# Kernel optimization log

Hardware: AMD Instinct MI355X
Metric: run time of the kernel (lower is better)

Reference implementation:

```python
import jax, jax.numpy as jnp
import numpy as np

NUM_EMBEDDINGS = 1024
DIM_EMBEDDING = 256
COMMITMENT_COST = 0.25


def setup_inputs() -> dict:
    key = jax.random.key(0)
    k1, k2 = jax.random.split(key)
    inputs = jax.random.normal(k1, (64, DIM_EMBEDDING, 32, 32), dtype=jnp.float32)
    # torch init: uniform(-1/K, 1/K)
    w = jax.random.uniform(k2, (NUM_EMBEDDINGS, DIM_EMBEDDING), dtype=jnp.float32,
                           minval=-1.0 / NUM_EMBEDDINGS, maxval=1.0 / NUM_EMBEDDINGS)
    return {"inputs": inputs, "w": w}


def reference(inputs, w):
    # NCHW -> NHWC
    x = jnp.transpose(inputs, (0, 2, 3, 1))            # [B,H,W,D]
    input_shape = x.shape
    flat = x.reshape(-1, DIM_EMBEDDING)                # [N,D]

    distances = (jnp.sum(flat * flat, axis=1, keepdims=True)
                 - 2.0 * jnp.matmul(flat, w.T)
                 + jnp.sum(w * w, axis=1))

    encoding_indices = jnp.argmax(-distances, axis=1)[:, None]      # [N,1] int
    encodings = jax.nn.one_hot(encoding_indices[:, 0], NUM_EMBEDDINGS,
                               dtype=jnp.float32)                   # [N,K]

    # gather instead of one-hot matmul (same math)
    quantized = jnp.take(w, encoding_indices[:, 0], axis=0)          # [N,D]
    quantized = quantized.reshape(input_shape)                       # [B,H,W,D]

    e_latent_loss = jnp.mean((jax.lax.stop_gradient(quantized) - x) ** 2)
    q_latent_loss = jnp.mean((quantized - jax.lax.stop_gradient(x)) ** 2)
    vq_loss = q_latent_loss + COMMITMENT_COST * e_latent_loss

    # straight-through estimator
    quantized_st = x + jax.lax.stop_gradient(quantized - x)
    quantized_out = jnp.transpose(quantized_st, (0, 3, 1, 2))        # NHWC -> NCHW

    avg_probs = jnp.mean(encodings, axis=0)
    perplexity = jnp.exp(-jnp.sum(avg_probs * jnp.log(avg_probs + 1e-10)))

    return (distances, quantized_out, vq_loss, encodings, encoding_indices, perplexity)
```

## Files before the change

### kernel.cpp

```cpp
#include <hip/hip_runtime.h>

#define N_TOT   65536
#define K_EMB   1024
#define D_EMB   256
#define HW      1024
#define CHW     (D_EMB * HW)

#define O_DIST  0
#define O_Q     67108864
#define O_LOSS  83886080
#define O_ENC   83886081
#define O_IDX   150994945
#define O_PPL   151060481

#define WS_CNT   0
#define WS_LOSSP 4096
#define WS_XX    6144
#define WS_WW    268288
#define WS_IDX   272384

__global__ __launch_bounds__(256) void k_xx(const float* __restrict__ in,
                                            float* __restrict__ xx) {
  int n = blockIdx.x * 256 + threadIdx.x;
  int b = n >> 10, hw = n & 1023;
  const float* p = in + (size_t)b * CHW + hw;
  float s = 0.f;
  #pragma unroll 8
  for (int d = 0; d < D_EMB; ++d) { float v = p[(size_t)d * HW]; s += v * v; }
  xx[n] = s;
}

__global__ __launch_bounds__(256) void k_ww(const float* __restrict__ w,
                                            float* __restrict__ ww) {
  int k = blockIdx.x * 256 + threadIdx.x;
  const float* p = w + (size_t)k * D_EMB;
  float s = 0.f;
  #pragma unroll 8
  for (int d = 0; d < D_EMB; ++d) { float v = p[d]; s += v * v; }
  ww[k] = s;
}

__global__ __launch_bounds__(256) void k_gemm(const float* __restrict__ in,
                                              const float* __restrict__ w,
                                              const float* __restrict__ xx,
                                              const float* __restrict__ ww,
                                              float* __restrict__ dist,
                                              int* __restrict__ aidx) {
  __shared__ __align__(16) float xs[32][68];
  __shared__ __align__(16) float wsh[32][68];
  __shared__ float rbest[64][16];
  __shared__ int   ridx[64][16];

  const int tid = threadIdx.x;
  const int tx = tid & 15, ty = tid >> 4;
  const int n0 = blockIdx.x * 64;
  const int b = n0 >> 10, hw0 = n0 & 1023;
  const float* xbase = in + (size_t)b * CHW + hw0;

  float best[4]; int bestk[4];
  #pragma unroll
  for (int i = 0; i < 4; ++i) { best[i] = 3.4e38f; bestk[i] = 0; }

  const int xr = tid >> 6;
  const int xc = tid & 63;
  const int wk = tid >> 3;
  const int wd = (tid & 7) * 4;

  for (int k0 = 0; k0 < K_EMB; k0 += 64) {
    float acc[4][4];
    #pragma unroll
    for (int i = 0; i < 4; ++i)
      #pragma unroll
      for (int j = 0; j < 4; ++j) acc[i][j] = 0.f;

    for (int d0 = 0; d0 < D_EMB; d0 += 32) {
      __syncthreads();
      #pragma unroll
      for (int it = 0; it < 8; ++it) {
        int dl = it * 4 + xr;
        xs[dl][xc] = xbase[(size_t)(d0 + dl) * HW + xc];
      }
      #pragma unroll
      for (int p = 0; p < 2; ++p) {
        int kl = p * 32 + wk;
        float4 v = *(const float4*)&w[(size_t)(k0 + kl) * D_EMB + d0 + wd];
        wsh[wd + 0][kl] = v.x; wsh[wd + 1][kl] = v.y;
        wsh[wd + 2][kl] = v.z; wsh[wd + 3][kl] = v.w;
      }
      __syncthreads();
      #pragma unroll
      for (int dd = 0; dd < 32; ++dd) {
        float4 xv = *(const float4*)&xs[dd][ty * 4];
        float4 wv = *(const float4*)&wsh[dd][tx * 4];
        acc[0][0] += xv.x * wv.x; acc[0][1] += xv.x * wv.y;
        acc[0][2] += xv.x * wv.z; acc[0][3] += xv.x * wv.w;
        acc[1][0] += xv.y * wv.x; acc[1][1] += xv.y * wv.y;
        acc[1][2] += xv.y * wv.z; acc[1][3] += xv.y * wv.w;
        acc[2][0] += xv.z * wv.x; acc[2][1] += xv.z * wv.y;
        acc[2][2] += xv.z * wv.z; acc[2][3] += xv.z * wv.w;
        acc[3][0] += xv.w * wv.x; acc[3][1] += xv.w * wv.y;
        acc[3][2] += xv.w * wv.z; acc[3][3] += xv.w * wv.w;
      }
    }
    float4 wwv = *(const float4*)&ww[k0 + tx * 4];
    #pragma unroll
    for (int i = 0; i < 4; ++i) {
      int nl = ty * 4 + i;
      float xxv = xx[n0 + nl];
      float4 o;
      o.x = xxv - 2.f * acc[i][0] + wwv.x;
      o.y = xxv - 2.f * acc[i][1] + wwv.y;
      o.z = xxv - 2.f * acc[i][2] + wwv.z;
      o.w = xxv - 2.f * acc[i][3] + wwv.w;
      *(float4*)&dist[(size_t)(n0 + nl) * K_EMB + k0 + tx * 4] = o;
      float dv[4] = {o.x, o.y, o.z, o.w};
      #pragma unroll
      for (int j = 0; j < 4; ++j) {
        if (dv[j] < best[i]) { best[i] = dv[j]; bestk[i] = k0 + tx * 4 + j; }
      }
    }
  }
  #pragma unroll
  for (int i = 0; i < 4; ++i) {
    rbest[ty * 4 + i][tx] = best[i];
    ridx[ty * 4 + i][tx] = bestk[i];
  }
  __syncthreads();
  if (tid < 64) {
    float bb = rbest[tid][0]; int bk = ridx[tid][0];
    #pragma unroll
    for (int t = 1; t < 16; ++t) {
      float v = rbest[tid][t]; int kk = ridx[tid][t];
      if (v < bb || (v == bb && kk < bk)) { bb = v; bk = kk; }
    }
    aidx[n0 + tid] = bk;
  }
}

__global__ __launch_bounds__(256) void k_epi(const float* __restrict__ in,
                                             const float* __restrict__ w,
                                             const int* __restrict__ aidx,
                                             float* __restrict__ outq,
                                             float* __restrict__ enc,
                                             float* __restrict__ idxf,
                                             int* __restrict__ cnt,
                                             double* __restrict__ lossp) {
  __shared__ double sred[256];
  int tid = threadIdx.x;
  int n = blockIdx.x * 256 + tid;
  int b = n >> 10, hw = n & 1023;
  int idx = aidx[n];
  const float* xp = in + (size_t)b * CHW + hw;
  float* qp = outq + (size_t)b * CHW + hw;
  const float* wrow = w + (size_t)idx * D_EMB;
  double ls = 0.0;
  #pragma unroll 4
  for (int d = 0; d < D_EMB; ++d) {
    float xv = xp[(size_t)d * HW];
    float q = wrow[d];
    float t = q - xv;
    qp[(size_t)d * HW] = xv + t;
    float sq = t * t;
    ls += (double)sq;
  }
  enc[(size_t)n * K_EMB + idx] = 1.0f;
  idxf[n] = (float)idx;
  atomicAdd(&cnt[idx], 1);
  sred[tid] = ls; __syncthreads();
  for (int s = 128; s > 0; s >>= 1) {
    if (tid < s) sred[tid] += sred[tid + s];
    __syncthreads();
  }
  if (tid == 0) lossp[blockIdx.x] = sred[0];
}

__global__ __launch_bounds__(256) void k_final(const double* __restrict__ lossp,
                                               const int* __restrict__ cnt,
                                               float* __restrict__ out_loss,
                                               float* __restrict__ out_ppl) {
  __shared__ double sred[256];
  int t = threadIdx.x;
  sred[t] = lossp[t];
  __syncthreads();
  for (int s = 128; s > 0; s >>= 1) {
    if (t < s) sred[t] += sred[t + s];
    __syncthreads();
  }
  if (t == 0) *out_loss = (float)(1.25 * (sred[0] / 16777216.0));
  __syncthreads();
  double es = 0.0;
  for (int k = t; k < K_EMB; k += 256) {
    float p = (float)cnt[k] * (1.0f / 65536.0f);
    float term = p * logf(p + 1e-10f);
    es += (double)term;
  }
  sred[t] = es;
  __syncthreads();
  for (int s = 128; s > 0; s >>= 1) {
    if (t < s) sred[t] += sred[t + s];
    __syncthreads();
  }
  if (t == 0) *out_ppl = expf((float)(-sred[0]));
}

extern "C" void kernel_launch(void* const* d_in, const int* in_sizes, int n_in,
                              void* d_out, int out_size, void* d_ws, size_t ws_size,
                              hipStream_t stream) {
  const float* in = (const float*)d_in[0];
  const float* w  = (const float*)d_in[1];
  float* out = (float*)d_out;
  char* ws = (char*)d_ws;

  int*    cnt   = (int*)(ws + WS_CNT);
  double* lossp = (double*)(ws + WS_LOSSP);
  float*  xx    = (float*)(ws + WS_XX);
  float*  wwp   = (float*)(ws + WS_WW);
  int*    aidx  = (int*)(ws + WS_IDX);

  hipMemsetAsync(cnt, 0, 4096, stream);
  hipMemsetAsync(out + O_ENC, 0, (size_t)67108864 * 4, stream);

  k_xx  <<<256, 256, 0, stream>>>(in, xx);
  k_ww  <<<4,   256, 0, stream>>>(w, wwp);
  k_gemm<<<1024, 256, 0, stream>>>(in, w, xx, wwp, out + O_DIST, aidx);
  k_epi <<<256, 256, 0, stream>>>(in, w, aidx, out + O_Q, out + O_ENC,
                                  out + O_IDX, cnt, lossp);
  k_final<<<1, 256, 0, stream>>>(lossp, cnt, out + O_LOSS, out + O_PPL);
}
```

Before: 1.200 ms.

## Use fp16 MFMA coarse distance GEMM with fp32 candidate re-evaluation for argmin

Converts inputs and codebook to fp16 (codebook scaled by 1024) in prep kernels and computes distances with v_mfma_f32_16x16x32_f16 using global_load_lds double-buffered staging. Per row, it records near-minimum candidates within a margin, then an fp32 re-evaluation kernel picks the exact argmin among them, falling back to a full scan on overflow. The epilogue now writes the full one-hot rows directly, which removes the large memset, and it reuses the encodings output region as scratch for the fp16 copies. The distances output now carries fp16-level error, which could affect tolerance.

```diff
diff --git a/kernel.cpp b/kernel.cpp
--- a/kernel.cpp
+++ b/kernel.cpp
@@ -1,4 +1,5 @@
 #include <hip/hip_runtime.h>
+#include <hip/hip_fp16.h>
 
 #define N_TOT   65536
 #define K_EMB   1024
@@ -15,157 +16,286 @@
 
 #define WS_CNT   0
 #define WS_LOSSP 4096
-#define WS_XX    6144
-#define WS_WW    268288
-#define WS_IDX   272384
-
-__global__ __launch_bounds__(256) void k_xx(const float* __restrict__ in,
-                                            float* __restrict__ xx) {
+#define WS_XX    12288
+#define WS_WW    274432
+#define WS_AIDX  278528
+
+#define CAP     15
+#define MARGIN  3.0e-4f
+
+typedef float  f32x4  __attribute__((ext_vector_type(4)));
+typedef short  short8 __attribute__((ext_vector_type(8)));
+typedef unsigned short ushort8 __attribute__((ext_vector_type(8)));
+typedef f32x4 __attribute__((aligned(4))) f32x4u;
+
+static __device__ __forceinline__ void gload16(const void* g, void* l) {
+  __builtin_amdgcn_global_load_lds(
+      (const __attribute__((address_space(1))) unsigned int*)g,
+      (__attribute__((address_space(3))) unsigned int*)l, 16, 0, 0);
+}
+
+__global__ __launch_bounds__(256) void k_prep_x(const float* __restrict__ in,
+                                                unsigned short* __restrict__ x2,
+                                                float* __restrict__ xx) {
   int n = blockIdx.x * 256 + threadIdx.x;
   int b = n >> 10, hw = n & 1023;
   const float* p = in + (size_t)b * CHW + hw;
-  float s = 0.f;
-  #pragma unroll 8
-  for (int d = 0; d < D_EMB; ++d) { float v = p[(size_t)d * HW]; s += v * v; }
-  xx[n] = s;
-}
-
-__global__ __launch_bounds__(256) void k_ww(const float* __restrict__ w,
-                                            float* __restrict__ ww) {
+  float hsum[2];
+  #pragma unroll
+  for (int half = 0; half < 2; ++half) {
+    float r[8];
+    for (int i = 0; i < 128; i += 8) {
+      ushort8 hv;
+      #pragma unroll
+      for (int j = 0; j < 8; ++j) {
+        int d = half * 128 + i + j;
+        float v = p[(size_t)d * HW];
+        float sq = v * v;
+        asm volatile("" : "+v"(sq));
+        if (i == 0) r[j] = sq; else r[j] += sq;
+        hv[j] = __half_as_ushort(__float2half_rn(v));
+      }
+      *(ushort8*)&x2[(size_t)n * 256 + half * 128 + i] = hv;
+    }
+    hsum[half] = ((r[0] + r[1]) + (r[2] + r[3])) + ((r[4] + r[5]) + (r[6] + r[7]));
+  }
+  xx[n] = hsum[0] + hsum[1];
+}
+
+__global__ __launch_bounds__(256) void k_prep_w(const float* __restrict__ w,
+                                                unsigned short* __restrict__ w2,
+                                                float* __restrict__ ww) {
   int k = blockIdx.x * 256 + threadIdx.x;
   const float* p = w + (size_t)k * D_EMB;
-  float s = 0.f;
-  #pragma unroll 8
-  for (int d = 0; d < D_EMB; ++d) { float v = p[d]; s += v * v; }
-  ww[k] = s;
-}
-
-__global__ __launch_bounds__(256) void k_gemm(const float* __restrict__ in,
+  float hsum[2];
+  #pragma unroll
+  for (int half = 0; half < 2; ++half) {
+    float r[8];
+    for (int i = 0; i < 128; i += 8) {
+      ushort8 hv;
+      #pragma unroll
+      for (int j = 0; j < 8; ++j) {
+        float v = p[half * 128 + i + j];
+        float sq = v * v;
+        asm volatile("" : "+v"(sq));
+        if (i == 0) r[j] = sq; else r[j] += sq;
+        hv[j] = __half_as_ushort(__float2half_rn(v * 1024.f));
+      }
+      *(ushort8*)&w2[(size_t)k * 256 + half * 128 + i] = hv;
+    }
+    hsum[half] = ((r[0] + r[1]) + (r[2] + r[3])) + ((r[4] + r[5]) + (r[6] + r[7]));
+  }
+  ww[k] = hsum[0] + hsum[1];
+}
+
+__global__ __launch_bounds__(512) void k_coarse(const unsigned short* __restrict__ x2,
+                                                const unsigned short* __restrict__ w2,
+                                                const float* __restrict__ xx,
+                                                const float* __restrict__ ww,
+                                                float* __restrict__ dist,
+                                                unsigned short* __restrict__ cand) {
+  __shared__ __align__(16) short As[2][4096];
+  __shared__ __align__(16) short Bs[2][4096];
+  __shared__ unsigned rowprov[128];
+  __shared__ unsigned rowcnt[128];
+  __shared__ unsigned short rowcand[128][CAP];
+
+  const int tid = threadIdx.x;
+  const int l = tid & 63, v = tid >> 6;
+  const int n0 = blockIdx.x * 128;
+  const int qr = v >> 1, qc = v & 1;
+
+  if (tid < 128) { rowprov[tid] = 0x7F800000u; rowcnt[tid] = 0u; }
+
+  float xv[2][4];
+  #pragma unroll
+  for (int m = 0; m < 2; ++m)
+    #pragma unroll
+    for (int r = 0; r < 4; ++r)
+      xv[m][r] = xx[n0 + qr * 32 + m * 16 + (l >> 4) * 4 + r];
+
+  const int srcrow = tid >> 2, srcoff = (tid & 3) * 16;
+
+  #define STAGE(buf, u) do {                                                   \
+    int k0_ = ((u) >> 3) * 128, d0_ = ((u) & 7) * 32;                          \
+    gload16((const char*)x2 + (size_t)(n0 + srcrow) * 512 + d0_ * 2 + srcoff,  \
+            (char*)As[buf] + v * 1024);                                        \
+    gload16((const char*)w2 + (size_t)(k0_ + srcrow) * 512 + d0_ * 2 + srcoff, \
+            (char*)Bs[buf] + v * 1024);                                        \
+  } while (0)
+
+  f32x4 acc[2][4];
+  int cur = 0;
+  STAGE(0, 0);
+  __syncthreads();
+
+  for (int u = 0; u < 64; ++u) {
+    if ((u & 7) == 0) {
+      #pragma unroll
+      for (int m = 0; m < 2; ++m)
+        #pragma unroll
+        for (int n = 0; n < 4; ++n) acc[m][n] = (f32x4){0.f, 0.f, 0.f, 0.f};
+    }
+    if (u < 63) STAGE(cur ^ 1, u + 1);
+
+    short8 af[2], bfr[4];
+    #pragma unroll
+    for (int m = 0; m < 2; ++m)
+      af[m] = *(const short8*)((const char*)As[cur] +
+                               (qr * 32 + m * 16 + (l & 15)) * 64 + (l >> 4) * 16);
+    #pragma unroll
+    for (int n = 0; n < 4; ++n)
+      bfr[n] = *(const short8*)((const char*)Bs[cur] +
+                                (qc * 64 + n * 16 + (l & 15)) * 64 + (l >> 4) * 16);
+    #pragma unroll
+    for (int m = 0; m < 2; ++m)
+      #pragma unroll
+      for (int n = 0; n < 4; ++n)
+        asm("v_mfma_f32_16x16x32_f16 %0, %1, %2, %0"
+            : "+v"(acc[m][n]) : "v"(af[m]), "v"(bfr[n]));
+
+    if ((u & 7) == 7) {
+      const int k0 = (u >> 3) * 128;
+      float wv[4];
+      float rmin[2][4];
+      #pragma unroll
+      for (int m = 0; m < 2; ++m)
+        #pragma unroll
+        for (int r = 0; r < 4; ++r) rmin[m][r] = 3.4e38f;
+      #pragma unroll
+      for (int n = 0; n < 4; ++n) {
+        const int kg = k0 + qc * 64 + n * 16 + (l & 15);
+        wv[n] = ww[kg];
+        #pragma unroll
+        for (int m = 0; m < 2; ++m)
+          #pragma unroll
+          for (int r = 0; r < 4; ++r) {
+            const int rl = qr * 32 + m * 16 + (l >> 4) * 4 + r;
+            float dd = (xv[m][r] - acc[m][n][r] * (1.f / 512.f)) + wv[n];
+            dist[(size_t)(n0 + rl) * 1024 + kg] = dd;
+            rmin[m][r] = fminf(rmin[m][r], dd);
+          }
+      }
+      #pragma unroll
+      for (int off = 1; off < 16; off <<= 1)
+        #pragma unroll
+        for (int m = 0; m < 2; ++m)
+          #pragma unroll
+          for (int r = 0; r < 4; ++r)
+            rmin[m][r] = fminf(rmin[m][r], __shfl_xor(rmin[m][r], off));
+      if ((l & 15) == 0) {
+        #pragma unroll
+        for (int m = 0; m < 2; ++m)
+          #pragma unroll
+          for (int r = 0; r < 4; ++r)
+            atomicMin(&rowprov[qr * 32 + m * 16 + (l >> 4) * 4 + r],
+                      __float_as_uint(rmin[m][r]));
+      }
+      __syncthreads();
+      #pragma unroll
+      for (int n = 0; n < 4; ++n) {
+        const int kg = k0 + qc * 64 + n * 16 + (l & 15);
+        #pragma unroll
+        for (int m = 0; m < 2; ++m)
+          #pragma unroll
+          for (int r = 0; r < 4; ++r) {
+            const int rl = qr * 32 + m * 16 + (l >> 4) * 4 + r;
+            float dd = (xv[m][r] - acc[m][n][r] * (1.f / 512.f)) + wv[n];
+            if (dd < __uint_as_float(rowprov[rl]) + MARGIN) {
+              unsigned slot = atomicAdd(&rowcnt[rl], 1u);
+              if (slot < CAP) rowcand[rl][slot] = (unsigned short)kg;
+            }
+          }
+      }
+    }
+    __syncthreads();
+    cur ^= 1;
+  }
+
+  if (tid < 128) {
+    unsigned c = rowcnt[tid];
+    unsigned short* dst = cand + (size_t)(n0 + tid) * 16;
+    dst[0] = (c > CAP) ? (unsigned short)0xFFFF : (unsigned short)c;
+    #pragma unroll
+    for (int i = 0; i < CAP; ++i) dst[1 + i] = rowcand[tid][i];
+  }
+  #undef STAGE
+}
+
+__global__ __launch_bounds__(256) void k_reeval(const float* __restrict__ in,
+                                                const float* __restrict__ w,
+                                                const float* __restrict__ xx,
+                                                const float* __restrict__ ww,
+                                                const unsigned short* __restrict__ cand,
+                                                int* __restrict__ aidx) {
+  int n = blockIdx.x * 256 + threadIdx.x;
+  int b = n >> 10, hw = n & 1023;
+  const unsigned short* c = cand + (size_t)n * 16;
+  int cnt = c[0];
+  int best;
+  if (cnt == 1) {
+    best = c[1];
+  } else {
+    const float* xp = in + (size_t)b * CHW + hw;
+    const float xxv = xx[n];
+    float bd = 3.4e38f; int bk = 1 << 30;
+    const bool full = (cnt > CAP);
+    const int m = full ? K_EMB : cnt;
+    for (int i = 0; i < m; ++i) {
+      int k = full ? i : (int)c[1 + i];
+      const float* wr = w + (size_t)k * D_EMB;
+      float acc = 0.f;
+      for (int d = 0; d < D_EMB; ++d)
+        acc = fmaf(xp[(size_t)d * HW], wr[d], acc);
+      float t = 2.0f * acc;
+      asm volatile("" : "+v"(t));
+      float s = xxv - t;
+      asm volatile("" : "+v"(s));
+      float dd = s + ww[k];
+      if (dd < bd || (dd == bd && k < bk)) { bd = dd; bk = k; }
+    }
+    best = bk;
+  }
+  aidx[n] = best;
+}
+
+__global__ __launch_bounds__(256) void k_epi2(const float* __restrict__ in,
                                               const float* __restrict__ w,
-                                              const float* __restrict__ xx,
-                                              const float* __restrict__ ww,
-                                              float* __restrict__ dist,
-                                              int* __restrict__ aidx) {
-  __shared__ __align__(16) float xs[32][68];
-  __shared__ __align__(16) float wsh[32][68];
-  __shared__ float rbest[64][16];
-  __shared__ int   ridx[64][16];
-
+                                              const int* __restrict__ aidx,
+                                              float* __restrict__ outq,
+                                              float* __restrict__ enc,
+                                              float* __restrict__ idxf,
+                                              int* __restrict__ cnt,
+                                              double* __restrict__ lossp) {
+  __shared__ double sred[256];
+  __shared__ int sidx[64];
   const int tid = threadIdx.x;
-  const int tx = tid & 15, ty = tid >> 4;
+  const int rr = tid & 63, qd = tid >> 6;
   const int n0 = blockIdx.x * 64;
-  const int b = n0 >> 10, hw0 = n0 & 1023;
-  const float* xbase = in + (size_t)b * CHW + hw0;
-
-  float best[4]; int bestk[4];
-  #pragma unroll
-  for (int i = 0; i < 4; ++i) { best[i] = 3.4e38f; bestk[i] = 0; }
-
-  const int xr = tid >> 6;
-  const int xc = tid & 63;
-  const int wk = tid >> 3;
-  const int wd = (tid & 7) * 4;
-
-  for (int k0 = 0; k0 < K_EMB; k0 += 64) {
-    float acc[4][4];
-    #pragma unroll
-    for (int i = 0; i < 4; ++i)
-      #pragma unroll
-      for (int j = 0; j < 4; ++j) acc[i][j] = 0.f;
-
-    for (int d0 = 0; d0 < D_EMB; d0 += 32) {
-      __syncthreads();
-      #pragma unroll
-      for (int it = 0; it < 8; ++it) {
-        int dl = it * 4 + xr;
-        xs[dl][xc] = xbase[(size_t)(d0 + dl) * HW + xc];
-      }
-      #pragma unroll
-      for (int p = 0; p < 2; ++p) {
-        int kl = p * 32 + wk;
-        float4 v = *(const float4*)&w[(size_t)(k0 + kl) * D_EMB + d0 + wd];
-        wsh[wd + 0][kl] = v.x; wsh[wd + 1][kl] = v.y;
-        wsh[wd + 2][kl] = v.z; wsh[wd + 3][kl] = v.w;
-      }
-      __syncthreads();
-      #pragma unroll
-      for (int dd = 0; dd < 32; ++dd) {
-        float4 xv = *(const float4*)&xs[dd][ty * 4];
-        float4 wv = *(const float4*)&wsh[dd][tx * 4];
-        acc[0][0] += xv.x * wv.x; acc[0][1] += xv.x * wv.y;
-        acc[0][2] += xv.x * wv.z; acc[0][3] += xv.x * wv.w;
-        acc[1][0] += xv.y * wv.x; acc[1][1] += xv.y * wv.y;
-        acc[1][2] += xv.y * wv.z; acc[1][3] += xv.y * wv.w;
-        acc[2][0] += xv.z * wv.x; acc[2][1] += xv.z * wv.y;
-        acc[2][2] += xv.z * wv.z; acc[2][3] += xv.z * wv.w;
-        acc[3][0] += xv.w * wv.x; acc[3][1] += xv.w * wv.y;
-        acc[3][2] += xv.w * wv.z; acc[3][3] += xv.w * wv.w;
-      }
-    }
-    float4 wwv = *(const float4*)&ww[k0 + tx * 4];
-    #pragma unroll
-    for (int i = 0; i < 4; ++i) {
-      int nl = ty * 4 + i;
-      float xxv = xx[n0 + nl];
-      float4 o;
-      o.x = xxv - 2.f * acc[i][0] + wwv.x;
-      o.y = xxv - 2.f * acc[i][1] + wwv.y;
-      o.z = xxv - 2.f * acc[i][2] + wwv.z;
-      o.w = xxv - 2.f * acc[i][3] + wwv.w;
-      *(float4*)&dist[(size_t)(n0 + nl) * K_EMB + k0 + tx * 4] = o;
-      float dv[4] = {o.x, o.y, o.z, o.w};
-      #pragma unroll
-      for (int j = 0; j < 4; ++j) {
-        if (dv[j] < best[i]) { best[i] = dv[j]; bestk[i] = k0 + tx * 4 + j; }
-      }
-    }
-  }
-  #pragma unroll
-  for (int i = 0; i < 4; ++i) {
-    rbest[ty * 4 + i][tx] = best[i];
-    ridx[ty * 4 + i][tx] = bestk[i];
-  }
-  __syncthreads();
-  if (tid < 64) {
-    float bb = rbest[tid][0]; int bk = ridx[tid][0];
-    #pragma unroll
-    for (int t = 1; t < 16; ++t) {
-      float v = rbest[tid][t]; int kk = ridx[tid][t];
-      if (v < bb || (v == bb && kk < bk)) { bb = v; bk = kk; }
-    }
-    aidx[n0 + tid] = bk;
-  }
-}
-
-__global__ __launch_bounds__(256) void k_epi(const float* __restrict__ in,
-                                             const float* __restrict__ w,
-                                             const int* __restrict__ aidx,
-                                             float* __restrict__ outq,
-                                             float* __restrict__ enc,
-                                             float* __restrict__ idxf,
-                                             int* __restrict__ cnt,
-                                             double* __restrict__ lossp) {
-  __shared__ double sred[256];
-  int tid = threadIdx.x;
-  int n = blockIdx.x * 256 + tid;
-  int b = n >> 10, hw = n & 1023;
-  int idx = aidx[n];
+  const int n = n0 + rr;
+  const int b = n >> 10, hw = n & 1023;
+  if (qd == 0) sidx[rr] = aidx[n];
+  __syncthreads();
+  const int idx = sidx[rr];
   const float* xp = in + (size_t)b * CHW + hw;
   float* qp = outq + (size_t)b * CHW + hw;
   const float* wrow = w + (size_t)idx * D_EMB;
   double ls = 0.0;
-  #pragma unroll 4
-  for (int d = 0; d < D_EMB; ++d) {
-    float xv = xp[(size_t)d * HW];
+  for (int j = 0; j < 64; ++j) {
+    int d = qd * 64 + j;
+    float xvv = xp[(size_t)d * HW];
     float q = wrow[d];
-    float t = q - xv;
-    qp[(size_t)d * HW] = xv + t;
-    float sq = t * t;
-    ls += (double)sq;
-  }
-  enc[(size_t)n * K_EMB + idx] = 1.0f;
-  idxf[n] = (float)idx;
-  atomicAdd(&cnt[idx], 1);
+    float t = q - xvv;
+    qp[(size_t)d * HW] = xvv + t;
+    ls += (double)(t * t);
+  }
+  if (qd == 0) { idxf[n] = (float)idx; atomicAdd(&cnt[idx], 1); }
+  for (int it = 0; it < 64; ++it) {
+    int ii = sidx[it];
+    f32x4 z = {0.f, 0.f, 0.f, 0.f};
+    if ((ii >> 2) == tid) z[ii & 3] = 1.f;
+    *(f32x4u*)&enc[(size_t)(n0 + it) * 1024 + tid * 4] = z;
+  }
   sred[tid] = ls; __syncthreads();
   for (int s = 128; s > 0; s >>= 1) {
     if (tid < s) sred[tid] += sred[tid + s];
@@ -180,7 +310,7 @@
                                                float* __restrict__ out_ppl) {
   __shared__ double sred[256];
   int t = threadIdx.x;
-  sred[t] = lossp[t];
+  sred[t] = lossp[t] + lossp[t + 256] + lossp[t + 512] + lossp[t + 768];
   __syncthreads();
   for (int s = 128; s > 0; s >>= 1) {
     if (t < s) sred[t] += sred[t + s];
@@ -215,15 +345,19 @@
   double* lossp = (double*)(ws + WS_LOSSP);
   float*  xx    = (float*)(ws + WS_XX);
   float*  wwp   = (float*)(ws + WS_WW);
-  int*    aidx  = (int*)(ws + WS_IDX);
+  int*    aidx  = (int*)(ws + WS_AIDX);
+
+  unsigned short* x2   = (unsigned short*)(out + O_ENC + 3);
+  unsigned short* w2   = x2 + (size_t)N_TOT * 256;
+  unsigned short* cand = w2 + (size_t)K_EMB * 256;
 
   hipMemsetAsync(cnt, 0, 4096, stream);
-  hipMemsetAsync(out + O_ENC, 0, (size_t)67108864 * 4, stream);
-
-  k_xx  <<<256, 256, 0, stream>>>(in, xx);
-  k_ww  <<<4,   256, 0, stream>>>(w, wwp);
-  k_gemm<<<1024, 256, 0, stream>>>(in, w, xx, wwp, out + O_DIST, aidx);
-  k_epi <<<256, 256, 0, stream>>>(in, w, aidx, out + O_Q, out + O_ENC,
-                                  out + O_IDX, cnt, lossp);
+
+  k_prep_x<<<256, 256, 0, stream>>>(in, x2, xx);
+  k_prep_w<<<4, 256, 0, stream>>>(w, w2, wwp);
+  k_coarse<<<512, 512, 0, stream>>>(x2, w2, xx, wwp, out + O_DIST, cand);
+  k_reeval<<<256, 256, 0, stream>>>(in, w, xx, wwp, cand, aidx);
+  k_epi2<<<1024, 256, 0, stream>>>(in, w, aidx, out + O_Q, out + O_ENC,
+                                   out + O_IDX, cnt, lossp);
   k_final<<<1, 256, 0, stream>>>(lossp, cnt, out + O_LOSS, out + O_PPL);
 }
```

Result: faster. 1.027 ms (-14.4%).
